# Performance work log

Hardware: AMD Instinct MI355X
Metric: run time of the kernel (lower is better)

## Reference

```python
import jax, jax.numpy as jnp
import numpy as np

SAMPLE_RATE = 44100
N_HARMONICS = 60
B, T = 32, 64000


def setup_inputs() -> dict:
    key = jax.random.key(0)
    k1, k2, k3, k4 = jax.random.split(key, 4)
    f0 = jax.random.normal(k1, (B, T), dtype=jnp.float32)
    loudness = jax.random.uniform(k2, (B, T), dtype=jnp.float32)
    harmonic_mix = jax.random.uniform(k3, (B, T), dtype=jnp.float32)
    noise = jax.random.normal(k4, (B, T), dtype=jnp.float32)
    return {"f0": f0, "loudness": loudness, "harmonic_mix": harmonic_mix, "noise": noise}


def reference(f0, loudness, harmonic_mix, noise):
    # f0 (normalized log scale) -> Hz
    f0_hz = 20.0 * jnp.exp(f0)                                   # (B, T)
    # phase accumulation (sequential scan along time)
    phase_inc = 2.0 * jnp.pi * f0_hz / SAMPLE_RATE               # (B, T)
    phase = jnp.cumsum(phase_inc, axis=1)                        # (B, T)
    harmonics = jnp.arange(1, N_HARMONICS + 1, dtype=jnp.float32)  # (H,)
    # harmonic bank: sin(phase * k) weighted by 1/k, summed over k
    harmonic_phase = phase[:, :, None] * harmonics               # (B, T, H)
    harmonic_wave = jnp.einsum('bth,h->bt', jnp.sin(harmonic_phase), 1.0 / harmonics)
    harmonic_audio = harmonic_wave * loudness                    # (B, T)
    noise_audio = noise * loudness                               # (B, T)
    audio = harmonic_mix * harmonic_audio + (1.0 - harmonic_mix) * noise_audio
    peak = jnp.max(jnp.abs(audio), axis=1, keepdims=True)
    return audio / (peak + 1e-6)
```

## Files before the change

kernel.cpp:

```cpp
#include <hip/hip_runtime.h>
#include <math.h>

#define NROWS 32
#define TLEN  64000
#define NH    60
#define CPR   250
#define NCHUNK (NROWS * CPR)

#define C_REV (20.0f / 44100.0f)

__global__ __launch_bounds__(256) void red_kernel(const float* __restrict__ f0,
                                                  float* __restrict__ csum) {
    const int wid = threadIdx.x >> 6, lane = threadIdx.x & 63;
    const int chunk = blockIdx.x * 4 + wid;
    const float4 v = *reinterpret_cast<const float4*>(f0 + (size_t)chunk * 256 + lane * 4);
    float t = (__expf(v.x) + __expf(v.y) + __expf(v.z) + __expf(v.w)) * C_REV;
    #pragma unroll
    for (int off = 32; off; off >>= 1) t += __shfl_xor(t, off, 64);
    if (lane == 0) csum[chunk] = t;
}

__global__ __launch_bounds__(256) void base_kernel(const float* __restrict__ csum,
                                                   float* __restrict__ ubase) {
    __shared__ double wsum[4];
    const int row = blockIdx.x;
    const int t   = threadIdx.x;
    const int lane = t & 63, wid = t >> 6;
    double v = (t < CPR) ? (double)csum[row * CPR + t] : 0.0;
    double s = v;
    #pragma unroll
    for (int off = 1; off < 64; off <<= 1) {
        double u = __shfl_up(s, off, 64);
        if (lane >= off) s += u;
    }
    if (lane == 63) wsum[wid] = s;
    __syncthreads();
    double add = 0.0;
    #pragma unroll
    for (int w = 0; w < 3; ++w)
        if (w < wid) add += wsum[w];
    s += add;
    double e = s - v;
    e -= floor(e);
    if (t < CPR) ubase[row * CPR + t] = (float)e;
}

__global__ __launch_bounds__(256) void harm_kernel(const float* __restrict__ f0,
                                                   const float* __restrict__ loud,
                                                   const float* __restrict__ mixp,
                                                   const float* __restrict__ noise,
                                                   const float* __restrict__ ubase,
                                                   float* __restrict__ out,
                                                   float* __restrict__ wavemax) {
    const int wid = threadIdx.x >> 6, lane = threadIdx.x & 63;
    const int chunk = blockIdx.x * 4 + wid;
    const size_t i0 = (size_t)chunk * 256 + (size_t)lane * 4;

    const float4 f = *reinterpret_cast<const float4*>(f0 + i0);
    float p0 = __expf(f.x) * C_REV;
    float p1 = p0 + __expf(f.y) * C_REV;
    float p2 = p1 + __expf(f.z) * C_REV;
    float p3 = p2 + __expf(f.w) * C_REV;

    float s = p3;
    #pragma unroll
    for (int off = 1; off < 64; off <<= 1) {
        float u = __shfl_up(s, off, 64);
        if (lane >= off) s += u;
    }
    const float start = ubase[chunk] + (s - p3);

    float sk[4], skm1[4], c2[4], acc[4];
    const float pj[4] = {p0, p1, p2, p3};
    #pragma unroll
    for (int j = 0; j < 4; ++j) {
        float u = start + pj[j];
        u -= floorf(u);
        const float s1 = __builtin_amdgcn_sinf(u);
        c2[j]   = 2.0f * __builtin_amdgcn_cosf(u);
        sk[j]   = s1;
        skm1[j] = 0.0f;
        acc[j]  = s1;
    }
    #pragma unroll
    for (int k = 2; k <= NH; ++k) {
        #pragma unroll
        for (int j = 0; j < 4; ++j) {
            const float s1 = fmaf(c2[j], sk[j], -skm1[j]);
            skm1[j] = sk[j];
            sk[j]   = s1;
            acc[j]  = fmaf(s1, 1.0f / (float)k, acc[j]);
        }
    }

    const float4 L = *reinterpret_cast<const float4*>(loud  + i0);
    const float4 M = *reinterpret_cast<const float4*>(mixp  + i0);
    const float4 N = *reinterpret_cast<const float4*>(noise + i0);
    float4 a;
    a.x = M.x * (acc[0] * L.x) + (1.0f - M.x) * (N.x * L.x);
    a.y = M.y * (acc[1] * L.y) + (1.0f - M.y) * (N.y * L.y);
    a.z = M.z * (acc[2] * L.z) + (1.0f - M.z) * (N.z * L.z);
    a.w = M.w * (acc[3] * L.w) + (1.0f - M.w) * (N.w * L.w);
    *reinterpret_cast<float4*>(out + i0) = a;

    float v = fmaxf(fmaxf(fabsf(a.x), fabsf(a.y)), fmaxf(fabsf(a.z), fabsf(a.w)));
    #pragma unroll
    for (int off = 32; off; off >>= 1)
        v = fmaxf(v, __shfl_xor(v, off, 64));
    if (lane == 0) wavemax[chunk] = v;
}

__global__ __launch_bounds__(64) void maxred_kernel(const float* __restrict__ wavemax,
                                                    float* __restrict__ rowmax) {
    const int row = blockIdx.x, lane = threadIdx.x;
    float v = 0.0f;
    #pragma unroll
    for (int c = 0; c < 4; ++c) {
        const int idx = lane + c * 64;
        if (idx < CPR) v = fmaxf(v, wavemax[row * CPR + idx]);
    }
    #pragma unroll
    for (int off = 32; off; off >>= 1)
        v = fmaxf(v, __shfl_xor(v, off, 64));
    if (lane == 0) rowmax[row] = v;
}

__global__ __launch_bounds__(256) void norm_kernel(float* __restrict__ out,
                                                   const float* __restrict__ rowmax) {
    const size_t q = (size_t)blockIdx.x * blockDim.x + threadIdx.x;
    const size_t i = q * 4;
    const int row = (int)(i / TLEN);
    const float denom = rowmax[row] + 1e-6f;
    float4 v = *reinterpret_cast<float4*>(out + i);
    v.x /= denom; v.y /= denom; v.z /= denom; v.w /= denom;
    *reinterpret_cast<float4*>(out + i) = v;
}

extern "C" void kernel_launch(void* const* d_in, const int* in_sizes, int n_in,
                              void* d_out, int out_size, void* d_ws, size_t ws_size,
                              hipStream_t stream) {
    const float* f0    = (const float*)d_in[0];
    const float* loud  = (const float*)d_in[1];
    const float* mixp  = (const float*)d_in[2];
    const float* noise = (const float*)d_in[3];
    float* out = (float*)d_out;

    float* csum    = (float*)d_ws;
    float* ubase   = csum + NCHUNK;
    float* wavemax = ubase + NCHUNK;
    float* rowmax  = wavemax + NCHUNK;

    red_kernel   <<<NCHUNK / 4, 256, 0, stream>>>(f0, csum);
    base_kernel  <<<NROWS,      256, 0, stream>>>(csum, ubase);
    harm_kernel  <<<NCHUNK / 4, 256, 0, stream>>>(f0, loud, mixp, noise, ubase, out, wavemax);
    maxred_kernel<<<NROWS,      64,  0, stream>>>(wavemax, rowmax);
    norm_kernel  <<<2000,       256, 0, stream>>>(out, rowmax);
}
```

Baseline: 92.72 us.

## Fold row prefix and max reduction into neighbouring kernels, cutting launches

Drops the separate base_kernel that scanned chunk sums per row. Each wavefront in harm_kernel now sums the preceding chunk sums of its row in double precision itself. The separate row-max kernel is also removed: each norm_kernel wave recomputes its row max from the per-chunk maxima before scaling. This removes two small serial launches and their dependency gaps, at the cost of redundant reads and reductions (up to 250 values per wave), plus double-precision adds inside the main kernel.

```diff
diff --git a/kernel.cpp b/kernel.cpp
--- a/kernel.cpp
+++ b/kernel.cpp
@@ -20,41 +20,29 @@
     if (lane == 0) csum[chunk] = t;
 }
 
-__global__ __launch_bounds__(256) void base_kernel(const float* __restrict__ csum,
-                                                   float* __restrict__ ubase) {
-    __shared__ double wsum[4];
-    const int row = blockIdx.x;
-    const int t   = threadIdx.x;
-    const int lane = t & 63, wid = t >> 6;
-    double v = (t < CPR) ? (double)csum[row * CPR + t] : 0.0;
-    double s = v;
-    #pragma unroll
-    for (int off = 1; off < 64; off <<= 1) {
-        double u = __shfl_up(s, off, 64);
-        if (lane >= off) s += u;
-    }
-    if (lane == 63) wsum[wid] = s;
-    __syncthreads();
-    double add = 0.0;
-    #pragma unroll
-    for (int w = 0; w < 3; ++w)
-        if (w < wid) add += wsum[w];
-    s += add;
-    double e = s - v;
-    e -= floor(e);
-    if (t < CPR) ubase[row * CPR + t] = (float)e;
-}
-
 __global__ __launch_bounds__(256) void harm_kernel(const float* __restrict__ f0,
                                                    const float* __restrict__ loud,
                                                    const float* __restrict__ mixp,
                                                    const float* __restrict__ noise,
-                                                   const float* __restrict__ ubase,
+                                                   const float* __restrict__ csum,
                                                    float* __restrict__ out,
                                                    float* __restrict__ wavemax) {
     const int wid = threadIdx.x >> 6, lane = threadIdx.x & 63;
     const int chunk = blockIdx.x * 4 + wid;
+    const int row   = chunk / CPR;
+    const int cpos  = chunk - row * CPR;
     const size_t i0 = (size_t)chunk * 256 + (size_t)lane * 4;
+
+    double b = 0.0;
+    #pragma unroll
+    for (int c = 0; c < 4; ++c) {
+        const int idx = lane + c * 64;
+        if (idx < cpos) b += (double)csum[row * CPR + idx];
+    }
+    #pragma unroll
+    for (int off = 32; off; off >>= 1) b += __shfl_xor(b, off, 64);
+    b -= floor(b);
+    const float start0 = (float)b;
 
     const float4 f = *reinterpret_cast<const float4*>(f0 + i0);
     float p0 = __expf(f.x) * C_REV;
@@ -68,7 +56,7 @@
         float u = __shfl_up(s, off, 64);
         if (lane >= off) s += u;
     }
-    const float start = ubase[chunk] + (s - p3);
+    const float start = start0 + (s - p3);
 
     float sk[4], skm1[4], c2[4], acc[4];
     const float pj[4] = {p0, p1, p2, p3};
@@ -110,30 +98,27 @@
     if (lane == 0) wavemax[chunk] = v;
 }
 
-__global__ __launch_bounds__(64) void maxred_kernel(const float* __restrict__ wavemax,
-                                                    float* __restrict__ rowmax) {
-    const int row = blockIdx.x, lane = threadIdx.x;
-    float v = 0.0f;
+__global__ __launch_bounds__(64) void norm_kernel(float* __restrict__ out,
+                                                  const float* __restrict__ wavemax) {
+    const int chunk = blockIdx.x;
+    const int row   = chunk / CPR;
+    const int lane  = threadIdx.x;
+
+    float m = 0.0f;
     #pragma unroll
     for (int c = 0; c < 4; ++c) {
         const int idx = lane + c * 64;
-        if (idx < CPR) v = fmaxf(v, wavemax[row * CPR + idx]);
+        if (idx < CPR) m = fmaxf(m, wavemax[row * CPR + idx]);
     }
     #pragma unroll
     for (int off = 32; off; off >>= 1)
-        v = fmaxf(v, __shfl_xor(v, off, 64));
-    if (lane == 0) rowmax[row] = v;
-}
+        m = fmaxf(m, __shfl_xor(m, off, 64));
+    const float denom = m + 1e-6f;
 
-__global__ __launch_bounds__(256) void norm_kernel(float* __restrict__ out,
-                                                   const float* __restrict__ rowmax) {
-    const size_t q = (size_t)blockIdx.x * blockDim.x + threadIdx.x;
-    const size_t i = q * 4;
-    const int row = (int)(i / TLEN);
-    const float denom = rowmax[row] + 1e-6f;
-    float4 v = *reinterpret_cast<float4*>(out + i);
+    const size_t i0 = (size_t)chunk * 256 + (size_t)lane * 4;
+    float4 v = *reinterpret_cast<float4*>(out + i0);
     v.x /= denom; v.y /= denom; v.z /= denom; v.w /= denom;
-    *reinterpret_cast<float4*>(out + i) = v;
+    *reinterpret_cast<float4*>(out + i0) = v;
 }
 
 extern "C" void kernel_launch(void* const* d_in, const int* in_sizes, int n_in,
@@ -146,13 +131,9 @@
     float* out = (float*)d_out;
 
     float* csum    = (float*)d_ws;
-    float* ubase   = csum + NCHUNK;
-    float* wavemax = ubase + NCHUNK;
-    float* rowmax  = wavemax + NCHUNK;
+    float* wavemax = csum + NCHUNK;
 
-    red_kernel   <<<NCHUNK / 4, 256, 0, stream>>>(f0, csum);
-    base_kernel  <<<NROWS,      256, 0, stream>>>(csum, ubase);
-    harm_kernel  <<<NCHUNK / 4, 256, 0, stream>>>(f0, loud, mixp, noise, ubase, out, wavemax);
-    maxred_kernel<<<NROWS,      64,  0, stream>>>(wavemax, rowmax);
-    norm_kernel  <<<2000,       256, 0, stream>>>(out, rowmax);
+    red_kernel <<<NCHUNK / 4, 256, 0, stream>>>(f0, csum);
+    harm_kernel<<<NCHUNK / 4, 256, 0, stream>>>(f0, loud, mixp, noise, csum, out, wavemax);
+    norm_kernel<<<NCHUNK,     64,  0, stream>>>(out, wavemax);
 }
```

Result: no change. 91.20 us (-1.6%).
